# Kernel tuning notes

Measured on AMD Instinct MI355X. Metric: run time of the kernel, lower is better.

The kernel has to match this reference:

```python
import jax, jax.numpy as jnp
from jax import lax
import numpy as np

NPOINT = 2048
NSAMPLE = 16
LEAKY = 0.1


def _leaky(x):
    return jnp.where(x >= 0, x, LEAKY * x)


def _fps(pts, npoint):
    # pts: [B, N, 3] -> idx [B, npoint] (furthest point sampling, start at index 0)
    B, N, _ = pts.shape

    def step(carry, _):
        dist, far = carry  # dist [B,N], far [B]
        c = jnp.take_along_axis(pts, far[:, None, None], axis=1)  # [B,1,3]
        d = jnp.sum((pts - c) ** 2, -1)  # [B,N]
        dist = jnp.minimum(dist, d)
        nxt = jnp.argmax(dist, -1).astype(jnp.int32)
        return (dist, nxt), far

    init = (jnp.full((B, N), 1e10, pts.dtype), jnp.zeros((B,), jnp.int32))
    _, idx = lax.scan(step, init, None, length=npoint)
    return jnp.transpose(idx)  # [B, npoint]


def setup_inputs() -> dict:
    key = jax.random.key(0)
    ks = jax.random.split(key, 6)
    B, N, D, O = 8, 8192, 64, 128
    xyz = jax.random.normal(ks[0], (B, 3, N), jnp.float32)
    points = jax.random.normal(ks[1], (B, D, N), jnp.float32)
    W_kernel = jax.random.normal(ks[2], (O, D + 3), jnp.float32) * 0.05
    W_linear = jax.random.normal(ks[3], (O + NSAMPLE, O + NSAMPLE), jnp.float32) * 0.05
    W_point = jax.random.normal(ks[4], (NSAMPLE, NSAMPLE), jnp.float32) * 0.05
    W_channel = jax.random.normal(ks[5], (O, O), jnp.float32) * 0.05
    return {"xyz": xyz, "points": points, "W_kernel": W_kernel,
            "W_linear": W_linear, "W_point": W_point, "W_channel": W_channel}


def reference(xyz, points, W_kernel, W_linear, W_point, W_channel):
    K, S = NSAMPLE, NPOINT
    xyz_t = jnp.transpose(xyz, (0, 2, 1))      # [B,N,3]
    pts_t = jnp.transpose(points, (0, 2, 1))   # [B,N,D]

    fps_idx = _fps(xyz_t, S)                   # [B,S]
    new_xyz = jax.vmap(lambda p, i: p[i])(xyz_t, fps_idx)  # [B,S,3]

    # KNN: squared distances new_xyz -> xyz
    d = (jnp.sum(new_xyz ** 2, -1)[:, :, None]
         + jnp.sum(xyz_t ** 2, -1)[:, None, :]
         - 2.0 * jnp.einsum('bsc,bnc->bsn', new_xyz, xyz_t))  # [B,S,N]
    _, knn = lax.top_k(-d, K)                  # [B,S,K]

    gxyz = jax.vmap(lambda p, i: p[i])(xyz_t, knn)          # [B,S,K,3]
    gxyz_n = gxyz - new_xyz[:, :, None, :]
    gpts = jax.vmap(lambda p, i: p[i])(pts_t, knn)          # [B,S,K,D]
    new_points = jnp.concatenate([gxyz_n, gpts], -1)        # [B,S,K,3+D]

    # 1x1 conv2d kernel + LeakyReLU
    feat = _leaky(jnp.einsum('oc,bskc->bosk', W_kernel, new_points))  # [B,O,S,K]

    ch_avg = jnp.mean(feat, -1)                # [B,O,S]
    pt_avg = jnp.mean(feat, 1)                 # [B,S,K]
    agg = jnp.concatenate([ch_avg, jnp.transpose(pt_avg, (0, 2, 1))], 1)  # [B,O+K,S]
    agg = _leaky(jnp.einsum('oc,bcs->bos', W_linear, agg))

    wp = jax.nn.sigmoid(jnp.einsum('oc,bcs->bos', W_point, agg[:, -K:]))   # [B,K,S]
    wc = jax.nn.sigmoid(jnp.einsum('oc,bcs->bos', W_channel, agg[:, :-K]))  # [B,O,S]

    gated = feat * wc[:, :, :, None] * jnp.transpose(wp, (0, 2, 1))[:, None, :, :]
    out = jnp.mean(gated, -1)                  # [B,O,S]
    return jnp.transpose(new_xyz, (0, 2, 1)), out, fps_idx
```

## Files before the change

### kernel.cpp

```cpp
#include <hip/hip_runtime.h>
#include <stdint.h>

#define NB 8
#define NPT 8192
#define ND 64
#define NO 128
#define NS 2048
#define NK 16
#define NCONS 248
#define NITER 67

typedef float f32x2 __attribute__((ext_vector_type(2)));

constexpr int WS_PTS_T  = 0;
constexpr int WS_XYZW   = WS_PTS_T + NB*NPT*ND;
constexpr int WS_GFAR   = WS_XYZW + NB*NPT*4;
constexpr int WS_SYNC   = WS_GFAR + NB*NS;

constexpr int OUT_NEWXYZ = 0;
constexpr int OUT_FEAT   = NB*3*NS;
constexpr int OUT_FPS    = OUT_FEAT + NB*NO*NS;

__device__ __forceinline__ float sq3(float x, float y, float z) {
#pragma clang fp contract(off)
  return (x*x + y*y) + z*z;
}

__device__ __forceinline__ f32x2 fps_d2(f32x2 px, f32x2 py, f32x2 pz, f32x2 cx, f32x2 cy, f32x2 cz) {
#pragma clang fp contract(off)
  f32x2 dx = px - cx, dy = py - cy, dz = pz - cz;
  return (dx*dx + dy*dy) + dz*dz;
}

__device__ __forceinline__ float knn_d(float qn, float pn,
                                       float qx,float qy,float qz,
                                       float px,float py,float pz) {
#pragma clang fp contract(off)
  float dot = (qx*px + qy*py) + qz*pz;
  return (qn + pn) - 2.0f*dot;
}

__device__ __forceinline__ float wave_max_dpp(float x) {
  int v;
  v = __builtin_amdgcn_update_dpp(__float_as_int(x), __float_as_int(x), 0x111, 0xF, 0xF, false);
  x = fmaxf(x, __int_as_float(v));
  v = __builtin_amdgcn_update_dpp(__float_as_int(x), __float_as_int(x), 0x112, 0xF, 0xF, false);
  x = fmaxf(x, __int_as_float(v));
  v = __builtin_amdgcn_update_dpp(__float_as_int(x), __float_as_int(x), 0x114, 0xF, 0xF, false);
  x = fmaxf(x, __int_as_float(v));
  v = __builtin_amdgcn_update_dpp(__float_as_int(x), __float_as_int(x), 0x118, 0xF, 0xF, false);
  x = fmaxf(x, __int_as_float(v));
  v = __builtin_amdgcn_update_dpp(__float_as_int(x), __float_as_int(x), 0x142, 0xA, 0xF, false);
  x = fmaxf(x, __int_as_float(v));
  v = __builtin_amdgcn_update_dpp(__float_as_int(x), __float_as_int(x), 0x143, 0xC, 0xF, false);
  x = fmaxf(x, __int_as_float(v));
  return x;
}

__device__ __forceinline__ float dpp8_max(float x) {
  int v;
  v = __builtin_amdgcn_update_dpp(__float_as_int(x), __float_as_int(x), 0x111, 0xF, 0xF, false);
  x = fmaxf(x, __int_as_float(v));
  v = __builtin_amdgcn_update_dpp(__float_as_int(x), __float_as_int(x), 0x112, 0xF, 0xF, false);
  x = fmaxf(x, __int_as_float(v));
  v = __builtin_amdgcn_update_dpp(__float_as_int(x), __float_as_int(x), 0x114, 0xF, 0xF, false);
  x = fmaxf(x, __int_as_float(v));
  return x;
}

__global__ void k_init(float* __restrict__ ws) {
  int idx = blockIdx.x*512 + threadIdx.x;
  if (idx < NB*NS) ((int*)(ws + WS_GFAR))[idx] = -1;
  if (idx < 32)    ((int*)(ws + WS_SYNC))[idx] = 0;
}

struct MegaShared {
  union {
    struct {
      float lxyz[NPT][4];
      unsigned long long wred[2][8];
      int farbuf[64];
    } f;
    struct { float tile[64][65]; } tr;
    struct {
      float W[128*69];
      union {
        float dist[NPT];
        struct { float np[16*69]; float ft[16*132]; float chred[256]; float ptred[16*17]; } p2;
      } u;
      unsigned long long kred[8];
      int selIdx[16];
      float agg[144];
      float a2[144];
      float gates[144];
      int farSlot;
    } c;
  } u;
};

__global__ __launch_bounds__(512) void k_mega(const float* __restrict__ xyz,
                                              const float* __restrict__ points,
                                              const float* __restrict__ Wkern,
                                              const float* __restrict__ Wlin,
                                              const float* __restrict__ Wpt,
                                              const float* __restrict__ Wch,
                                              float* __restrict__ ws,
                                              float* __restrict__ dout) {
  __shared__ MegaShared sh;
  const int bid = blockIdx.x, t = threadIdx.x;
  int* syncp = (int*)(ws + WS_SYNC);
  int* gfar  = (int*)(ws + WS_GFAR);

  if (bid < NB) {
    const float* xb = xyz + (size_t)bid*3*NPT;
    f32x2 px2[8], py2[8], pz2[8], dist2[8];
    const int base = t << 4;
#pragma unroll
    for (int jj = 0; jj < 4; jj++) {
      float4 vx = *reinterpret_cast<const float4*>(xb + base + jj*4);
      float4 vy = *reinterpret_cast<const float4*>(xb + NPT + base + jj*4);
      float4 vz = *reinterpret_cast<const float4*>(xb + 2*NPT + base + jj*4);
      px2[jj*2+0] = f32x2{vx.x, vx.y}; px2[jj*2+1] = f32x2{vx.z, vx.w};
      py2[jj*2+0] = f32x2{vy.x, vy.y}; py2[jj*2+1] = f32x2{vy.z, vy.w};
      pz2[jj*2+0] = f32x2{vz.x, vz.y}; pz2[jj*2+1] = f32x2{vz.z, vz.w};
      dist2[jj*2+0] = f32x2{1e10f, 1e10f}; dist2[jj*2+1] = f32x2{1e10f, 1e10f};
      float xs[4] = {vx.x, vx.y, vx.z, vx.w};
      float ys[4] = {vy.x, vy.y, vy.z, vy.w};
      float zs[4] = {vz.x, vz.y, vz.z, vz.w};
#pragma unroll
      for (int i = 0; i < 4; i++) {
        float4 rec; rec.x = xs[i]; rec.y = ys[i]; rec.z = zs[i]; rec.w = 0.f;
        *reinterpret_cast<float4*>(&sh.u.f.lxyz[base + jj*4 + i][0]) = rec;
      }
    }
    __syncthreads();

    int far = 0;
    int* gfb = gfar + (size_t)bid*NS;

    for (int s = 0; s < NS; s++) {
      if (t == 480) sh.u.f.farbuf[s & 63] = far;
      if ((s & 31) == 0 && s > 0 && (t >> 6) == 1) {
        int l = t & 63;
        if (l < 32) {
          int q = s - 32 + l;
          int fq = sh.u.f.farbuf[q & 63];
          __hip_atomic_store(&gfb[q], fq, __ATOMIC_RELAXED, __HIP_MEMORY_SCOPE_AGENT);
        }
      }

      const float4 c4 = *reinterpret_cast<const float4*>(&sh.u.f.lxyz[far][0]);
      const f32x2 c2x = {c4.x, c4.x}, c2y = {c4.y, c4.y}, c2z = {c4.z, c4.z};

      f32x2 vmax2 = {-1.0f, -1.0f};
#pragma unroll
      for (int j = 0; j < 8; j++) {
        f32x2 dd = fps_d2(px2[j], py2[j], pz2[j], c2x, c2y, c2z);
        f32x2 nd;
        nd.x = fminf(dist2[j].x, dd.x);
        nd.y = fminf(dist2[j].y, dd.y);
        dist2[j] = nd;
        vmax2.x = fmaxf(vmax2.x, nd.x);
        vmax2.y = fmaxf(vmax2.y, nd.y);
      }
      float bv = fmaxf(vmax2.x, vmax2.y);
      int bi = base;
#pragma unroll
      for (int j = 7; j >= 0; --j) {
        if (dist2[j].y == bv) bi = base + 2*j + 1;
        if (dist2[j].x == bv) bi = base + 2*j;
      }
      float wm = wave_max_dpp(bv);
      float wmax = __int_as_float(__builtin_amdgcn_readlane(__float_as_int(wm), 63));
      unsigned long long eq = __ballot(bv == wmax);
      int winner = __ffsll((unsigned long long)eq) - 1;
      int wbi = __builtin_amdgcn_readlane(bi, winner);
      const int par = s & 1;
      if ((t & 63) == 0)
        sh.u.f.wred[par][t >> 6] = ((unsigned long long)__float_as_uint(wmax) << 32) | (unsigned)wbi;
      __syncthreads();
      {
        unsigned long long kk = sh.u.f.wred[par][t & 7];
        float sv = __int_as_float((int)(unsigned)(kk >> 32));
        float sm = dpp8_max(sv);
        float M = __int_as_float(__builtin_amdgcn_readlane(__float_as_int(sm), 7));
        unsigned long long eqm = __ballot(sv == M) & 0xFFull;
        int wwin = __ffsll(eqm) - 1;
        far = __builtin_amdgcn_readlane((int)(kk & 0xFFFFFFFFull), wwin);
      }
    }
    if ((t >> 6) == 1) {
      int l = t & 63;
      if (l < 32) {
        int q = NS - 32 + l;
        int fq = sh.u.f.farbuf[q & 63];
        __hip_atomic_store(&gfb[q], fq, __ATOMIC_RELAXED, __HIP_MEMORY_SCOPE_AGENT);
      }
    }
    return;
  }

  const int cbid = bid - NB;

  for (int tile = cbid; tile < 1024; tile += NCONS) {
    const int b  = tile >> 7;
    const int n0 = (tile & 127) << 6;
    const float* pb = points + (size_t)b*ND*NPT;
    {
      int dR = t >> 3, cg = t & 7;
      const float* src = pb + (size_t)dR*NPT + n0 + cg*8;
      float4 v0 = *reinterpret_cast<const float4*>(src);
      float4 v1 = *reinterpret_cast<const float4*>(src + 4);
      sh.u.tr.tile[dR][cg*8+0]=v0.x; sh.u.tr.tile[dR][cg*8+1]=v0.y;
      sh.u.tr.tile[dR][cg*8+2]=v0.z; sh.u.tr.tile[dR][cg*8+3]=v0.w;
      sh.u.tr.tile[dR][cg*8+4]=v1.x; sh.u.tr.tile[dR][cg*8+5]=v1.y;
      sh.u.tr.tile[dR][cg*8+6]=v1.z; sh.u.tr.tile[dR][cg*8+7]=v1.w;
    }
    __syncthreads();
    {
      int nl = t >> 3, dg = t & 7;
      float4 w0, w1;
      w0.x = sh.u.tr.tile[dg*8+0][nl]; w0.y = sh.u.tr.tile[dg*8+1][nl];
      w0.z = sh.u.tr.tile[dg*8+2][nl]; w0.w = sh.u.tr.tile[dg*8+3][nl];
      w1.x = sh.u.tr.tile[dg*8+4][nl]; w1.y = sh.u.tr.tile[dg*8+5][nl];
      w1.z = sh.u.tr.tile[dg*8+6][nl]; w1.w = sh.u.tr.tile[dg*8+7][nl];
      float* dst = ws + WS_PTS_T + ((size_t)b*NPT + n0 + nl)*ND + dg*8;
      *reinterpret_cast<float4*>(dst)     = w0;
      *reinterpret_cast<float4*>(dst + 4) = w1;
    }
    __syncthreads();
  }
  for (int chunk = cbid; chunk < 128; chunk += NCONS) {
    int g = chunk*512 + t;
    int b = g >> 13, n = g & 8191;
    const float* xb = xyz + (size_t)b*3*NPT;
    float x = xb[n], y = xb[NPT+n], z = xb[2*NPT+n];
    float4 v; v.x=x; v.y=y; v.z=z; v.w=sq3(x,y,z);
    *reinterpret_cast<float4*>(ws + WS_XYZW + (size_t)g*4) = v;
  }
  __syncthreads();
  if (t == 0) {
    __hip_atomic_fetch_add(&syncp[0], 1, __ATOMIC_ACQ_REL, __HIP_MEMORY_SCOPE_AGENT);
    while (__hip_atomic_load(&syncp[0], __ATOMIC_RELAXED, __HIP_MEMORY_SCOPE_AGENT) < NCONS)
      __builtin_amdgcn_s_sleep(8);
    (void)__hip_atomic_load(&syncp[0], __ATOMIC_ACQUIRE, __HIP_MEMORY_SCOPE_AGENT);
  }
  __syncthreads();

  for (int g = t; g < 128*67; g += 512) {
    int o = g / 67, c = g - o*67;
    sh.u.c.W[o*69+c] = Wkern[g];
  }
  __syncthreads();

  for (int j = 0; j < NITER; j++) {
    const int i = cbid + j*NCONS;
    const bool active = (i < NB*NS);
    const int ii = active ? i : (NB*NS - 1);
    const int b = ii & 7, s = ii >> 3;

    if (t == 0) {
      int f;
      while ((f = __hip_atomic_load(&gfar[(size_t)b*NS + s], __ATOMIC_RELAXED, __HIP_MEMORY_SCOPE_AGENT)) == -1)
        __builtin_amdgcn_s_sleep(8);
      sh.u.c.farSlot = f;
    }
    __syncthreads();
    const int far = sh.u.c.farSlot;

    const float* xyzw = ws + WS_XYZW + (size_t)b*NPT*4;
    const float4 q = *reinterpret_cast<const float4*>(xyzw + (size_t)far*4);

    if (active) {
      if (t == 3) dout[OUT_FPS + (size_t)b*NS + s] = (float)far;
      else if (t < 3) dout[OUT_NEWXYZ + (size_t)b*3*NS + (size_t)t*NS + s] = (t==0) ? q.x : (t==1) ? q.y : q.z;
    }

#pragma unroll
    for (int i2 = 0; i2 < 16; i2++) {
      int n = t + (i2 << 9);
      float4 p = *reinterpret_cast<const float4*>(xyzw + (size_t)n*4);
      sh.u.c.u.dist[n] = knn_d(q.w, p.w, q.x, q.y, q.z, p.x, p.y, p.z);
    }
    __syncthreads();

    for (int r = 0; r < NK; r++) {
      float bv = __int_as_float(0x7F800000); int bi = NPT;
#pragma unroll
      for (int i2 = 0; i2 < 16; i2++) {
        int n = t + (i2 << 9);
        float v = sh.u.c.u.dist[n];
        if (v < bv) { bv = v; bi = n; }
      }
      unsigned uu = __float_as_uint(bv);
      uu ^= ((unsigned)((int)uu >> 31)) | 0x80000000u;
      unsigned long long key = ((unsigned long long)uu << 32) | (unsigned)bi;
#pragma unroll
      for (int m = 1; m < 64; m <<= 1) {
        unsigned long long o = __shfl_xor(key, m, 64);
        key = (o < key) ? o : key;
      }
      if ((t & 63) == 0) sh.u.c.kred[t >> 6] = key;
      __syncthreads();
      if (t == 0) {
        unsigned long long kmin = sh.u.c.kred[0];
#pragma unroll
        for (int w = 1; w < 8; w++) { unsigned long long o = sh.u.c.kred[w]; if (o < kmin) kmin = o; }
        int win = (int)(kmin & 0xFFFFFFFFull);
        sh.u.c.selIdx[r] = win;
        sh.u.c.u.dist[win] = __int_as_float(0x7F800000);
      }
      __syncthreads();
    }

    if (t < 256) {
      int k = t >> 4, cg = t & 15;
      int idx = sh.u.c.selIdx[k];
      float4 f = *reinterpret_cast<const float4*>(ws + WS_PTS_T + ((size_t)b*NPT + idx)*ND + cg*4);
      float* nprow = sh.u.c.u.p2.np + k*69;
      nprow[3+cg*4+0]=f.x; nprow[3+cg*4+1]=f.y; nprow[3+cg*4+2]=f.z; nprow[3+cg*4+3]=f.w;
      if (cg == 0) {
        float4 g4 = *reinterpret_cast<const float4*>(xyzw + (size_t)idx*4);
        nprow[0]=g4.x-q.x; nprow[1]=g4.y-q.y; nprow[2]=g4.z-q.z;
      }
    }
    __syncthreads();

    if (t < 256) {
      const int o = t & 127, khalf = t >> 7, k0 = khalf*8;
      float acc[8] = {0,0,0,0,0,0,0,0};
      const float* Wrow = sh.u.c.W + o*69;
      for (int c = 0; c < 67; c++) {
        float w = Wrow[c];
#pragma unroll
        for (int kk = 0; kk < 8; kk++)
          acc[kk] = fmaf(w, sh.u.c.u.p2.np[(k0+kk)*69 + c], acc[kk]);
      }
      float chp = 0.f;
#pragma unroll
      for (int kk = 0; kk < 8; kk++) {
        float a = acc[kk]; a = (a >= 0.f) ? a : 0.1f*a;
        sh.u.c.u.p2.ft[(k0+kk)*132 + o] = a; chp += a;
      }
      sh.u.c.u.p2.chred[khalf*128 + o] = chp;
    }
    __syncthreads();

    if (t < 128) sh.u.c.agg[t] = (sh.u.c.u.p2.chred[t] + sh.u.c.u.p2.chred[128+t]) * 0.0625f;
    if (t < 256) {
      int k = t & 15, og = t >> 4;
      float pp = 0.f;
#pragma unroll
      for (int jj = 0; jj < 8; jj++) pp += sh.u.c.u.p2.ft[k*132 + og*8 + jj];
      sh.u.c.u.p2.ptred[k*17 + og] = pp;
    }
    __syncthreads();
    if (t < 16) {
      float pv = 0.f;
#pragma unroll
      for (int og = 0; og < 16; og++) pv += sh.u.c.u.p2.ptred[t*17 + og];
      sh.u.c.agg[128 + t] = pv * 0.0078125f;
    }
    __syncthreads();

    if (t < 144) {
      float a = 0.f;
      const float* wr = Wlin + t*144;
      for (int c = 0; c < 144; c++) a = fmaf(wr[c], sh.u.c.agg[c], a);
      sh.u.c.a2[t] = (a >= 0.f) ? a : 0.1f*a;
    }
    __syncthreads();

    if (t < 128) {
      float a = 0.f;
      const float* wr = Wch + t*128;
      for (int c = 0; c < 128; c++) a = fmaf(wr[c], sh.u.c.a2[c], a);
      sh.u.c.gates[t] = 1.f / (1.f + expf(-a));
    } else if (t < 144) {
      int o = t - 128;
      float a = 0.f;
      const float* wr = Wpt + o*16;
      for (int c = 0; c < 16; c++) a = fmaf(wr[c], sh.u.c.a2[128+c], a);
      sh.u.c.gates[t] = 1.f / (1.f + expf(-a));
    }
    __syncthreads();

    if (t < 128 && active) {
      float sum = 0.f;
#pragma unroll
      for (int k = 0; k < 16; k++)
        sum = fmaf(sh.u.c.u.p2.ft[k*132 + t], sh.u.c.gates[128 + k], sum);
      dout[OUT_FEAT + ((size_t)b*NO + t)*NS + s] = sum * sh.u.c.gates[t] * 0.0625f;
    }
    __syncthreads();
  }
}

extern "C" void kernel_launch(void* const* d_in, const int* in_sizes, int n_in,
                              void* d_out, int out_size, void* d_ws, size_t ws_size,
                              hipStream_t stream) {
  (void)in_sizes; (void)n_in; (void)out_size; (void)ws_size;
  const float* xyz    = (const float*)d_in[0];
  const float* points = (const float*)d_in[1];
  const float* Wk     = (const float*)d_in[2];
  const float* Wl     = (const float*)d_in[3];
  const float* Wp     = (const float*)d_in[4];
  const float* Wc     = (const float*)d_in[5];
  float* ws  = (float*)d_ws;
  float* out = (float*)d_out;

  hipLaunchKernelGGL(k_init, dim3(32), dim3(512), 0, stream, ws);

  void* args[] = { (void*)&xyz, (void*)&points, (void*)&Wk, (void*)&Wl,
                   (void*)&Wp, (void*)&Wc, (void*)&ws, (void*)&out };
  hipLaunchCooperativeKernel(reinterpret_cast<void*>(k_mega),
                             dim3(NB + NCONS), dim3(512), args, 0, stream);
}
```

Baseline: 1.965 ms.

## Morton-sort FPS points per thread and skip updates via bounding-box bound

In the furthest-point-sampling blocks, points are binned into an 8x8x8 Morton grid and counting-sorted in shared memory, so each thread owns a spatially compact set of 16 points with a tight bounding box. Each step, a thread compares the lower-bound distance from the new centre to its box against its cached max and skips the distance update when no point can change. Ties are broken toward the original lowest index with an unsigned-max DPP reduction in place of the ballot/ffs path. This removes most per-step ALU work in exchange for a sort prologue and a per-step global load of the centre. The 1.0002 slack on the bound is meant to keep the skip test conservative against rounding.

```diff
diff --git a/kernel.cpp b/kernel.cpp
--- a/kernel.cpp
+++ b/kernel.cpp
@@ -40,32 +40,52 @@
   return (qn + pn) - 2.0f*dot;
 }
 
+#define DPP_STEP_F(x, ctrl, rm, bm, op) { \
+  int _v = __builtin_amdgcn_update_dpp(__float_as_int(x), __float_as_int(x), ctrl, rm, bm, false); \
+  x = op(x, __int_as_float(_v)); }
+
 __device__ __forceinline__ float wave_max_dpp(float x) {
-  int v;
-  v = __builtin_amdgcn_update_dpp(__float_as_int(x), __float_as_int(x), 0x111, 0xF, 0xF, false);
-  x = fmaxf(x, __int_as_float(v));
-  v = __builtin_amdgcn_update_dpp(__float_as_int(x), __float_as_int(x), 0x112, 0xF, 0xF, false);
-  x = fmaxf(x, __int_as_float(v));
-  v = __builtin_amdgcn_update_dpp(__float_as_int(x), __float_as_int(x), 0x114, 0xF, 0xF, false);
-  x = fmaxf(x, __int_as_float(v));
-  v = __builtin_amdgcn_update_dpp(__float_as_int(x), __float_as_int(x), 0x118, 0xF, 0xF, false);
-  x = fmaxf(x, __int_as_float(v));
-  v = __builtin_amdgcn_update_dpp(__float_as_int(x), __float_as_int(x), 0x142, 0xA, 0xF, false);
-  x = fmaxf(x, __int_as_float(v));
-  v = __builtin_amdgcn_update_dpp(__float_as_int(x), __float_as_int(x), 0x143, 0xC, 0xF, false);
-  x = fmaxf(x, __int_as_float(v));
+  DPP_STEP_F(x, 0x111, 0xF, 0xF, fmaxf)
+  DPP_STEP_F(x, 0x112, 0xF, 0xF, fmaxf)
+  DPP_STEP_F(x, 0x114, 0xF, 0xF, fmaxf)
+  DPP_STEP_F(x, 0x118, 0xF, 0xF, fmaxf)
+  DPP_STEP_F(x, 0x142, 0xA, 0xF, fmaxf)
+  DPP_STEP_F(x, 0x143, 0xC, 0xF, fmaxf)
   return x;
 }
-
+__device__ __forceinline__ float wave_min_dpp(float x) {
+  DPP_STEP_F(x, 0x111, 0xF, 0xF, fminf)
+  DPP_STEP_F(x, 0x112, 0xF, 0xF, fminf)
+  DPP_STEP_F(x, 0x114, 0xF, 0xF, fminf)
+  DPP_STEP_F(x, 0x118, 0xF, 0xF, fminf)
+  DPP_STEP_F(x, 0x142, 0xA, 0xF, fminf)
+  DPP_STEP_F(x, 0x143, 0xC, 0xF, fminf)
+  return x;
+}
+__device__ __forceinline__ unsigned wave_umax_dpp(unsigned x) {
+#define DPP_STEP_U(ctrl, rm) { \
+  unsigned _v = (unsigned)__builtin_amdgcn_update_dpp((int)x, (int)x, ctrl, rm, 0xF, false); \
+  x = (x > _v) ? x : _v; }
+  DPP_STEP_U(0x111, 0xF) DPP_STEP_U(0x112, 0xF) DPP_STEP_U(0x114, 0xF)
+  DPP_STEP_U(0x118, 0xF) DPP_STEP_U(0x142, 0xA) DPP_STEP_U(0x143, 0xC)
+  return x;
+}
 __device__ __forceinline__ float dpp8_max(float x) {
-  int v;
-  v = __builtin_amdgcn_update_dpp(__float_as_int(x), __float_as_int(x), 0x111, 0xF, 0xF, false);
-  x = fmaxf(x, __int_as_float(v));
-  v = __builtin_amdgcn_update_dpp(__float_as_int(x), __float_as_int(x), 0x112, 0xF, 0xF, false);
-  x = fmaxf(x, __int_as_float(v));
-  v = __builtin_amdgcn_update_dpp(__float_as_int(x), __float_as_int(x), 0x114, 0xF, 0xF, false);
-  x = fmaxf(x, __int_as_float(v));
+  DPP_STEP_F(x, 0x111, 0xF, 0xF, fmaxf)
+  DPP_STEP_F(x, 0x112, 0xF, 0xF, fmaxf)
+  DPP_STEP_F(x, 0x114, 0xF, 0xF, fmaxf)
   return x;
+}
+__device__ __forceinline__ unsigned dpp8_umax(unsigned x) {
+  DPP_STEP_U(0x111, 0xF) DPP_STEP_U(0x112, 0xF) DPP_STEP_U(0x114, 0xF)
+  return x;
+}
+
+__device__ __forceinline__ unsigned morton3(unsigned x, unsigned y, unsigned z) {
+  unsigned m = (x & 1) | ((y & 1) << 1) | ((z & 1) << 2);
+  m |= ((x & 2) << 2) | ((y & 2) << 3) | ((z & 2) << 4);
+  m |= ((x & 4) << 4) | ((y & 4) << 5) | ((z & 4) << 6);
+  return m;
 }
 
 __global__ void k_init(float* __restrict__ ws) {
@@ -77,7 +97,11 @@
 struct MegaShared {
   union {
     struct {
-      float lxyz[NPT][4];
+      float lxyzo[NPT][4];
+      int hist[512];
+      int tmp[512];
+      int cs[512];
+      float bb[8][6];
       unsigned long long wred[2][8];
       int farbuf[64];
     } f;
@@ -113,88 +137,164 @@
 
   if (bid < NB) {
     const float* xb = xyz + (size_t)bid*3*NPT;
-    f32x2 px2[8], py2[8], pz2[8], dist2[8];
     const int base = t << 4;
+    const int w = t >> 6;
+
+    float lx[16], ly[16], lz[16];
 #pragma unroll
     for (int jj = 0; jj < 4; jj++) {
       float4 vx = *reinterpret_cast<const float4*>(xb + base + jj*4);
       float4 vy = *reinterpret_cast<const float4*>(xb + NPT + base + jj*4);
       float4 vz = *reinterpret_cast<const float4*>(xb + 2*NPT + base + jj*4);
-      px2[jj*2+0] = f32x2{vx.x, vx.y}; px2[jj*2+1] = f32x2{vx.z, vx.w};
-      py2[jj*2+0] = f32x2{vy.x, vy.y}; py2[jj*2+1] = f32x2{vy.z, vy.w};
-      pz2[jj*2+0] = f32x2{vz.x, vz.y}; pz2[jj*2+1] = f32x2{vz.z, vz.w};
-      dist2[jj*2+0] = f32x2{1e10f, 1e10f}; dist2[jj*2+1] = f32x2{1e10f, 1e10f};
-      float xs[4] = {vx.x, vx.y, vx.z, vx.w};
-      float ys[4] = {vy.x, vy.y, vy.z, vy.w};
-      float zs[4] = {vz.x, vz.y, vz.z, vz.w};
-#pragma unroll
-      for (int i = 0; i < 4; i++) {
-        float4 rec; rec.x = xs[i]; rec.y = ys[i]; rec.z = zs[i]; rec.w = 0.f;
-        *reinterpret_cast<float4*>(&sh.u.f.lxyz[base + jj*4 + i][0]) = rec;
-      }
-    }
-    __syncthreads();
+      lx[jj*4+0]=vx.x; lx[jj*4+1]=vx.y; lx[jj*4+2]=vx.z; lx[jj*4+3]=vx.w;
+      ly[jj*4+0]=vy.x; ly[jj*4+1]=vy.y; ly[jj*4+2]=vy.z; ly[jj*4+3]=vy.w;
+      lz[jj*4+0]=vz.x; lz[jj*4+1]=vz.y; lz[jj*4+2]=vz.z; lz[jj*4+3]=vz.w;
+    }
+    float mnx=lx[0],mxx=lx[0],mny=ly[0],mxy=ly[0],mnz=lz[0],mxz=lz[0];
+#pragma unroll
+    for (int j = 1; j < 16; j++) {
+      mnx=fminf(mnx,lx[j]); mxx=fmaxf(mxx,lx[j]);
+      mny=fminf(mny,ly[j]); mxy=fmaxf(mxy,ly[j]);
+      mnz=fminf(mnz,lz[j]); mxz=fmaxf(mxz,lz[j]);
+    }
+    float rmnx=wave_min_dpp(mnx), rmxx=wave_max_dpp(mxx);
+    float rmny=wave_min_dpp(mny), rmxy=wave_max_dpp(mxy);
+    float rmnz=wave_min_dpp(mnz), rmxz=wave_max_dpp(mxz);
+    if ((t & 63) == 63) {
+      sh.u.f.bb[w][0]=rmnx; sh.u.f.bb[w][1]=rmxx;
+      sh.u.f.bb[w][2]=rmny; sh.u.f.bb[w][3]=rmxy;
+      sh.u.f.bb[w][4]=rmnz; sh.u.f.bb[w][5]=rmxz;
+    }
+    sh.u.f.hist[t & 511] = 0;
+    __syncthreads();
+    float Bmnx=sh.u.f.bb[0][0], Bmxx=sh.u.f.bb[0][1];
+    float Bmny=sh.u.f.bb[0][2], Bmxy=sh.u.f.bb[0][3];
+    float Bmnz=sh.u.f.bb[0][4], Bmxz=sh.u.f.bb[0][5];
+#pragma unroll
+    for (int ww = 1; ww < 8; ww++) {
+      Bmnx=fminf(Bmnx,sh.u.f.bb[ww][0]); Bmxx=fmaxf(Bmxx,sh.u.f.bb[ww][1]);
+      Bmny=fminf(Bmny,sh.u.f.bb[ww][2]); Bmxy=fmaxf(Bmxy,sh.u.f.bb[ww][3]);
+      Bmnz=fminf(Bmnz,sh.u.f.bb[ww][4]); Bmxz=fmaxf(Bmxz,sh.u.f.bb[ww][5]);
+    }
+    float wx=Bmxx-Bmnx, wy=Bmxy-Bmny, wz=Bmxz-Bmnz;
+    float invx = (wx>0.f)?(8.0f/wx):0.f;
+    float invy = (wy>0.f)?(8.0f/wy):0.f;
+    float invz = (wz>0.f)?(8.0f/wz):0.f;
+    int cid[16];
+#pragma unroll
+    for (int j = 0; j < 16; j++) {
+      int cxi = min(7, (int)((lx[j]-Bmnx)*invx));
+      int cyi = min(7, (int)((ly[j]-Bmny)*invy));
+      int czi = min(7, (int)((lz[j]-Bmnz)*invz));
+      cid[j] = (int)morton3((unsigned)cxi,(unsigned)cyi,(unsigned)czi);
+      atomicAdd(&sh.u.f.hist[cid[j]], 1);
+    }
+    __syncthreads();
+    {
+      int* A = sh.u.f.hist; int* B = sh.u.f.tmp;
+      for (int d = 1; d < 512; d <<= 1) {
+        int v = A[t] + ((t >= d) ? A[t-d] : 0);
+        B[t] = v;
+        __syncthreads();
+        int* sw = A; A = B; B = sw;
+      }
+      sh.u.f.cs[t] = (t == 0) ? 0 : A[t-1];
+    }
+    __syncthreads();
+#pragma unroll
+    for (int j = 0; j < 16; j++) {
+      int pos = atomicAdd(&sh.u.f.cs[cid[j]], 1);
+      float4 rec; rec.x=lx[j]; rec.y=ly[j]; rec.z=lz[j]; rec.w=__int_as_float(base+j);
+      *reinterpret_cast<float4*>(&sh.u.f.lxyzo[pos][0]) = rec;
+    }
+    __syncthreads();
+    f32x2 px2[8], py2[8], pz2[8], dist2[8];
+    unsigned oi[16];
+    float bmnx= 3e38f,bmxx=-3e38f,bmny= 3e38f,bmxy=-3e38f,bmnz= 3e38f,bmxz=-3e38f;
+#pragma unroll
+    for (int j = 0; j < 16; j++) {
+      float4 r = *reinterpret_cast<const float4*>(&sh.u.f.lxyzo[base + j][0]);
+      if (j & 1) { px2[j>>1].y=r.x; py2[j>>1].y=r.y; pz2[j>>1].y=r.z; }
+      else       { px2[j>>1].x=r.x; py2[j>>1].x=r.y; pz2[j>>1].x=r.z; }
+      oi[j] = (unsigned)__float_as_int(r.w);
+      bmnx=fminf(bmnx,r.x); bmxx=fmaxf(bmxx,r.x);
+      bmny=fminf(bmny,r.y); bmxy=fmaxf(bmxy,r.y);
+      bmnz=fminf(bmnz,r.z); bmxz=fmaxf(bmxz,r.z);
+    }
+#pragma unroll
+    for (int j = 0; j < 8; j++) dist2[j] = f32x2{1e10f, 1e10f};
+    float cachedMax = 3e38f; unsigned cachedCand = 0;
 
     int far = 0;
     int* gfb = gfar + (size_t)bid*NS;
 
     for (int s = 0; s < NS; s++) {
       if (t == 480) sh.u.f.farbuf[s & 63] = far;
-      if ((s & 31) == 0 && s > 0 && (t >> 6) == 1) {
+      if ((s & 31) == 0 && s > 0 && w == 1) {
         int l = t & 63;
         if (l < 32) {
           int q = s - 32 + l;
-          int fq = sh.u.f.farbuf[q & 63];
-          __hip_atomic_store(&gfb[q], fq, __ATOMIC_RELAXED, __HIP_MEMORY_SCOPE_AGENT);
+          __hip_atomic_store(&gfb[q], sh.u.f.farbuf[q & 63], __ATOMIC_RELAXED, __HIP_MEMORY_SCOPE_AGENT);
         }
       }
-
-      const float4 c4 = *reinterpret_cast<const float4*>(&sh.u.f.lxyz[far][0]);
-      const f32x2 c2x = {c4.x, c4.x}, c2y = {c4.y, c4.y}, c2z = {c4.z, c4.z};
-
-      f32x2 vmax2 = {-1.0f, -1.0f};
-#pragma unroll
-      for (int j = 0; j < 8; j++) {
-        f32x2 dd = fps_d2(px2[j], py2[j], pz2[j], c2x, c2y, c2z);
-        f32x2 nd;
-        nd.x = fminf(dist2[j].x, dd.x);
-        nd.y = fminf(dist2[j].y, dd.y);
-        dist2[j] = nd;
-        vmax2.x = fmaxf(vmax2.x, nd.x);
-        vmax2.y = fmaxf(vmax2.y, nd.y);
-      }
-      float bv = fmaxf(vmax2.x, vmax2.y);
-      int bi = base;
-#pragma unroll
-      for (int j = 7; j >= 0; --j) {
-        if (dist2[j].y == bv) bi = base + 2*j + 1;
-        if (dist2[j].x == bv) bi = base + 2*j;
-      }
-      float wm = wave_max_dpp(bv);
-      float wmax = __int_as_float(__builtin_amdgcn_readlane(__float_as_int(wm), 63));
-      unsigned long long eq = __ballot(bv == wmax);
-      int winner = __ffsll((unsigned long long)eq) - 1;
-      int wbi = __builtin_amdgcn_readlane(bi, winner);
+      const int fr = far;
+      const float cx = xb[fr], cy = xb[NPT + fr], cz = xb[2*NPT + fr];
+
+      float ddx = fmaxf(fmaxf(bmnx - cx, cx - bmxx), 0.f);
+      float ddy = fmaxf(fmaxf(bmny - cy, cy - bmxy), 0.f);
+      float ddz = fmaxf(fmaxf(bmnz - cz, cz - bmxz), 0.f);
+      float lb2 = ddx*ddx + ddy*ddy + ddz*ddz;
+
+      float bv; unsigned cand;
+      if (lb2 <= cachedMax * 1.0002f) {
+        const f32x2 c2x = {cx, cx}, c2y = {cy, cy}, c2z = {cz, cz};
+        f32x2 vmax2 = {-1.0f, -1.0f};
+#pragma unroll
+        for (int j = 0; j < 8; j++) {
+          f32x2 dd = fps_d2(px2[j], py2[j], pz2[j], c2x, c2y, c2z);
+          f32x2 nd;
+          nd.x = fminf(dist2[j].x, dd.x);
+          nd.y = fminf(dist2[j].y, dd.y);
+          dist2[j] = nd;
+          vmax2.x = fmaxf(vmax2.x, nd.x);
+          vmax2.y = fmaxf(vmax2.y, nd.y);
+        }
+        bv = fmaxf(vmax2.x, vmax2.y);
+        cand = 0;
+#pragma unroll
+        for (int j = 0; j < 8; j++) {
+          unsigned sx = (dist2[j].x == bv) ? (8191u - oi[2*j])   : 0u;
+          unsigned sy = (dist2[j].y == bv) ? (8191u - oi[2*j+1]) : 0u;
+          unsigned m = (sx > sy) ? sx : sy;
+          cand = (cand > m) ? cand : m;
+        }
+        cachedMax = bv; cachedCand = cand;
+      } else {
+        bv = cachedMax; cand = cachedCand;
+      }
+      float wmv = wave_max_dpp(bv);
+      float wmax = __int_as_float(__builtin_amdgcn_readlane(__float_as_int(wmv), 63));
+      unsigned cnd = (bv == wmax) ? cand : 0u;
+      unsigned wcv = wave_umax_dpp(cnd);
+      unsigned wcand = (unsigned)__builtin_amdgcn_readlane((int)wcv, 63);
       const int par = s & 1;
       if ((t & 63) == 0)
-        sh.u.f.wred[par][t >> 6] = ((unsigned long long)__float_as_uint(wmax) << 32) | (unsigned)wbi;
+        sh.u.f.wred[par][w] = ((unsigned long long)__float_as_uint(wmax) << 32) | wcand;
       __syncthreads();
-      {
-        unsigned long long kk = sh.u.f.wred[par][t & 7];
-        float sv = __int_as_float((int)(unsigned)(kk >> 32));
-        float sm = dpp8_max(sv);
-        float M = __int_as_float(__builtin_amdgcn_readlane(__float_as_int(sm), 7));
-        unsigned long long eqm = __ballot(sv == M) & 0xFFull;
-        int wwin = __ffsll(eqm) - 1;
-        far = __builtin_amdgcn_readlane((int)(kk & 0xFFFFFFFFull), wwin);
-      }
-    }
-    if ((t >> 6) == 1) {
+      unsigned long long kk = sh.u.f.wred[par][t & 7];
+      float sv = __int_as_float((int)(unsigned)(kk >> 32));
+      float sm = dpp8_max(sv);
+      float M = __int_as_float(__builtin_amdgcn_readlane(__float_as_int(sm), 7));
+      unsigned c2v = (sv == M) ? (unsigned)(kk & 0xFFFFFFFFull) : 0u;
+      unsigned s2v = dpp8_umax(c2v);
+      unsigned W = (unsigned)__builtin_amdgcn_readlane((int)s2v, 7);
+      far = __builtin_amdgcn_readfirstlane(8191 - (int)W);
+    }
+    if (w == 1) {
       int l = t & 63;
       if (l < 32) {
         int q = NS - 32 + l;
-        int fq = sh.u.f.farbuf[q & 63];
-        __hip_atomic_store(&gfb[q], fq, __ATOMIC_RELAXED, __HIP_MEMORY_SCOPE_AGENT);
+        __hip_atomic_store(&gfb[q], sh.u.f.farbuf[q & 63], __ATOMIC_RELAXED, __HIP_MEMORY_SCOPE_AGENT);
       }
     }
     return;
@@ -305,7 +405,7 @@
       if (t == 0) {
         unsigned long long kmin = sh.u.c.kred[0];
 #pragma unroll
-        for (int w = 1; w < 8; w++) { unsigned long long o = sh.u.c.kred[w]; if (o < kmin) kmin = o; }
+        for (int w2 = 1; w2 < 8; w2++) { unsigned long long o = sh.u.c.kred[w2]; if (o < kmin) kmin = o; }
         int win = (int)(kmin & 0xFFFFFFFFull);
         sh.u.c.selIdx[r] = win;
         sh.u.c.u.dist[win] = __int_as_float(0x7F800000);
@@ -331,10 +431,10 @@
       float acc[8] = {0,0,0,0,0,0,0,0};
       const float* Wrow = sh.u.c.W + o*69;
       for (int c = 0; c < 67; c++) {
-        float w = Wrow[c];
+        float wv = Wrow[c];
 #pragma unroll
         for (int kk = 0; kk < 8; kk++)
-          acc[kk] = fmaf(w, sh.u.c.u.p2.np[(k0+kk)*69 + c], acc[kk]);
+          acc[kk] = fmaf(wv, sh.u.c.u.p2.np[(k0+kk)*69 + c], acc[kk]);
       }
       float chp = 0.f;
 #pragma unroll
```

Result: slower. 2.155 ms (+9.6%).
